# Optimization experiments

Hardware: AMD Instinct MI355X
Metric: run time of the kernel (lower is better)

Reference implementation:

```python
import jax, jax.numpy as jnp
import numpy as np

N = 50000        # nodes
E = 800000       # edges (before self loops)
G = 512          # graphs
H = 2            # heads
FIN = 128        # in_features
CH = 64          # hidden per head
COUT = 32        # out_features
NEG_SLOPE = 0.2  # PyG GATConv default
BN_EPS = 1e-5


def _gat(x, src, dst, W, a_src, a_dst, b, concat, n):
    # x: [n, F], W: [F, H*C], a_src/a_dst: [H, C]
    h = (x @ W).reshape(n, a_src.shape[0], a_src.shape[1])        # [n, H, C]
    e = jax.nn.leaky_relu((h * a_src).sum(-1)[src]
                          + (h * a_dst).sum(-1)[dst], NEG_SLOPE)  # [Etot, H]
    # per-destination segment softmax (self loops guarantee nonempty segments)
    m = jax.ops.segment_max(e, dst, num_segments=n)
    ex = jnp.exp(e - m[dst])
    s = jax.ops.segment_sum(ex, dst, num_segments=n)
    alpha = ex / (s[dst] + 1e-16)                                 # [Etot, H]
    out = jax.ops.segment_sum(h[src] * alpha[:, :, None], dst, num_segments=n)
    out = out.reshape(n, -1) if concat else out.mean(axis=1)
    return out + b


def _bn(x, gamma, beta, mean, var):
    # BatchNorm1d in eval mode (running statistics)
    return (x - mean) * jax.lax.rsqrt(var + BN_EPS) * gamma + beta


def setup_inputs() -> dict:
    key = jax.random.key(0)
    ks = jax.random.split(key, 12)
    x = jax.random.normal(ks[0], (N, FIN), dtype=jnp.float32)
    edge_index = jax.random.randint(ks[1], (2, E), 0, N, dtype=jnp.int32)
    batch = jnp.sort(jax.random.randint(ks[2], (N,), 0, G, dtype=jnp.int32))
    inp = {"x": x, "edge_index": edge_index, "batch": batch}
    # layer 1: GATConv(FIN -> CH, heads=H, concat=True)
    inp["W1"] = jax.random.normal(ks[3], (FIN, H * CH), dtype=jnp.float32) * 0.1
    inp["as1"] = jax.random.normal(ks[4], (H, CH), dtype=jnp.float32) * 0.1
    inp["ad1"] = jax.random.normal(ks[5], (H, CH), dtype=jnp.float32) * 0.1
    inp["b1"] = jnp.zeros((H * CH,), dtype=jnp.float32)
    inp["bn1_gamma"] = jnp.ones((H * CH,), dtype=jnp.float32)
    inp["bn1_beta"] = jnp.zeros((H * CH,), dtype=jnp.float32)
    inp["bn1_mean"] = jax.random.normal(ks[6], (H * CH,), dtype=jnp.float32) * 0.05
    inp["bn1_var"] = jnp.ones((H * CH,), dtype=jnp.float32)
    # layer 2: GATConv(H*CH -> COUT, heads=H, concat=False)
    inp["W2"] = jax.random.normal(ks[7], (H * CH, H * COUT), dtype=jnp.float32) * 0.1
    inp["as2"] = jax.random.normal(ks[8], (H, COUT), dtype=jnp.float32) * 0.1
    inp["ad2"] = jax.random.normal(ks[9], (H, COUT), dtype=jnp.float32) * 0.1
    inp["b2"] = jnp.zeros((COUT,), dtype=jnp.float32)
    inp["bn2_gamma"] = jnp.ones((COUT,), dtype=jnp.float32)
    inp["bn2_beta"] = jnp.zeros((COUT,), dtype=jnp.float32)
    inp["bn2_mean"] = jax.random.normal(ks[10], (COUT,), dtype=jnp.float32) * 0.05
    inp["bn2_var"] = jnp.ones((COUT,), dtype=jnp.float32)
    return inp


def reference(x, edge_index, batch,
              W1, as1, ad1, b1, bn1_gamma, bn1_beta, bn1_mean, bn1_var,
              W2, as2, ad2, b2, bn2_gamma, bn2_beta, bn2_mean, bn2_var):
    n = x.shape[0]
    sl = jnp.arange(n, dtype=edge_index.dtype)
    src = jnp.concatenate([edge_index[0], sl])  # PyG add_self_loops=True
    dst = jnp.concatenate([edge_index[1], sl])
    h = _gat(x, src, dst, W1, as1, ad1, b1, True, n)
    h = jax.nn.relu(_bn(h, bn1_gamma, bn1_beta, bn1_mean, bn1_var))
    h = _gat(h, src, dst, W2, as2, ad2, b2, False, n)
    h = _bn(h, bn2_gamma, bn2_beta, bn2_mean, bn2_var)
    # global mean pool over graphs
    sums = jax.ops.segment_sum(h, batch, num_segments=G)
    cnts = jax.ops.segment_sum(jnp.ones((n,), h.dtype), batch, num_segments=G)
    pooled = sums / jnp.maximum(cnts, 1.0)[:, None]
    return jax.nn.log_softmax(pooled, axis=1)
```

## Files before the change

### kernel.cpp

```cpp
#include <hip/hip_runtime.h>
#include <hip/hip_bf16.h>

#define NEG_SLOPE 0.2f
#define BN_EPS 1e-5f
#define BSHIFT 7
#define P_PART 256
#define MAXB 512

typedef unsigned int uint32;
typedef unsigned short ushort16;
typedef __attribute__((ext_vector_type(8))) short bf16x8;
typedef __attribute__((ext_vector_type(4))) float f32x4;

__device__ __forceinline__ ushort16 f2bf(float f) {
    uint32 u = __float_as_uint(f);
    u = (u + 0x7fff + ((u >> 16) & 1)) >> 16;
    return (ushort16)u;
}
__device__ __forceinline__ float bfu_lo(uint32 u) { return __uint_as_float(u << 16); }
__device__ __forceinline__ float bfu_hi(uint32 u) { return __uint_as_float(u & 0xffff0000u); }

__device__ __forceinline__ void scan_bbase(const int* __restrict__ rowtot, int nbuck,
                                           int Etot, int* sb ) {
    const int t = threadIdx.x;
    int v0 = (t < nbuck) ? rowtot[t] : 0;
    int v1 = (256 + t < nbuck) ? rowtot[256 + t] : 0;
    sb[t] = v0;
    sb[256 + t] = v1;
    __syncthreads();
    for (int off = 1; off < 512; off <<= 1) {
        int a0 = (t >= off) ? sb[t - off] : 0;
        int a1 = (256 + t >= off) ? sb[256 + t - off] : 0;
        __syncthreads();
        sb[t] += a0;
        sb[256 + t] += a1;
        __syncthreads();
    }
    int i0 = sb[t], i1 = sb[256 + t];
    __syncthreads();
    sb[t] = i0 - v0;
    sb[256 + t] = i1 - v1;
    if (t == 0) sb[MAXB] = Etot;
    __syncthreads();
}

template <int OC, int C>
__device__ __forceinline__ void pack_col(int col, int k, const float* __restrict__ W,
                                         const float* __restrict__ a_s,
                                         const float* __restrict__ a_d,
                                         ushort16* __restrict__ wt) {
    float v = 0.f;
    if (col < OC) {
        v = W[k * OC + col];
    } else if (col < OC + 2) {
        int hh = col - OC;
        float s = 0.f;
        for (int c = 0; c < C; ++c) s += W[k * OC + hh * C + c] * a_s[hh * C + c];
        v = s;
    } else if (col < OC + 4) {
        int hh = col - OC - 2;
        float s = 0.f;
        for (int c = 0; c < C; ++c) s += W[k * OC + hh * C + c] * a_d[hh * C + c];
        v = s;
    }
    wt[(size_t)col * 128 + k] = f2bf(v);
}

template <int OC, int NT, bool AF32>
__device__ __forceinline__ void gemm_body(int gb, const void* __restrict__ xin,
                                          const ushort16* __restrict__ wt,
                                          ushort16* __restrict__ h, float4* __restrict__ att,
                                          float2* __restrict__ asc, int N) {
    const int wave = threadIdx.x >> 6, lane = threadIdx.x & 63;
    const int tile = gb * 4 + wave;
    if (tile * 16 >= N) return;
    const int m = lane & 15, quad = lane >> 4;
    const int node = tile * 16 + m;

    bf16x8 a[4];
    if (AF32) {
        const float* xr = (const float*)xin + (size_t)node * 128 + quad * 8;
#pragma unroll
        for (int c = 0; c < 4; ++c) {
            float4 u = *(const float4*)(xr + c * 32);
            float4 v = *(const float4*)(xr + c * 32 + 4);
            bf16x8 t;
            t[0] = (short)f2bf(u.x); t[1] = (short)f2bf(u.y);
            t[2] = (short)f2bf(u.z); t[3] = (short)f2bf(u.w);
            t[4] = (short)f2bf(v.x); t[5] = (short)f2bf(v.y);
            t[6] = (short)f2bf(v.z); t[7] = (short)f2bf(v.w);
            a[c] = t;
        }
    } else {
        const ushort16* xr = (const ushort16*)xin + (size_t)node * 128 + quad * 8;
#pragma unroll
        for (int c = 0; c < 4; ++c) a[c] = *(const bf16x8*)(xr + c * 32);
    }

    for (int t = 0; t < NT; ++t) {
        const ushort16* wr = wt + ((size_t)(t * 16 + m)) * 128 + quad * 8;
        bf16x8 b[4];
#pragma unroll
        for (int c = 0; c < 4; ++c) b[c] = *(const bf16x8*)(wr + c * 32);
        f32x4 acc = {0.f, 0.f, 0.f, 0.f};
#pragma unroll
        for (int c = 0; c < 4; ++c)
            acc = __builtin_amdgcn_mfma_f32_16x16x32_bf16(a[c], b[c], acc, 0, 0, 0);
        if (t * 16 < OC) {
#pragma unroll
            for (int r = 0; r < 4; ++r) {
                int nrow = tile * 16 + quad * 4 + r;
                h[(size_t)nrow * OC + t * 16 + m] = f2bf(acc[r]);
            }
        } else if (m < 4) {
#pragma unroll
            for (int r = 0; r < 4; ++r) {
                int nrow = tile * 16 + quad * 4 + r;
                ((float*)(att + nrow))[m] = acc[r];
                if (m < 2) ((float*)(asc + nrow))[m] = acc[r];
            }
        }
    }
}

__global__ __launch_bounds__(256) void fused_prep(
    const int* __restrict__ ei, int E, int Etot, int nbuck, int chunk, int* __restrict__ hist,
    const float* __restrict__ W1, const float* __restrict__ as1, const float* __restrict__ ad1,
    ushort16* __restrict__ wt1,
    const float* __restrict__ W2, const float* __restrict__ as2, const float* __restrict__ ad2,
    ushort16* __restrict__ wt2,
    const int* __restrict__ batch, int N, int G, int* __restrict__ gstart) {
    const int bid = blockIdx.x;
    if (bid < P_PART) {
        __shared__ int lh[MAXB];
        const int p = bid;
        for (int i = threadIdx.x; i < nbuck; i += 256) lh[i] = 0;
        __syncthreads();
        const int beg = p * chunk;
        const int end = min(beg + chunk, Etot);
        for (int i = beg + threadIdx.x; i < end; i += 256) {
            int d = (i < E) ? ei[E + i] : i - E;
            atomicAdd(&lh[d >> BSHIFT], 1);
        }
        __syncthreads();
        for (int i = threadIdx.x; i < nbuck; i += 256) hist[(size_t)i * P_PART + p] = lh[i];
        return;
    }
    int rb = bid - P_PART;
    if (rb < 72) {
        pack_col<128, 64>(rb * 2 + (threadIdx.x >> 7), threadIdx.x & 127, W1, as1, ad1, wt1);
        return;
    }
    rb -= 72;
    if (rb < 40) {
        pack_col<64, 32>(rb * 2 + (threadIdx.x >> 7), threadIdx.x & 127, W2, as2, ad2, wt2);
        return;
    }
    rb -= 40;
    {
        int g = rb * 256 + (int)threadIdx.x;
        if (g > G) return;
        if (g == G) { gstart[G] = N; return; }
        int lo = 0, hi = N;
        while (lo < hi) { int mid = (lo + hi) >> 1; if (batch[mid] < g) lo = mid + 1; else hi = mid; }
        gstart[g] = lo;
    }
}

__global__ __launch_bounds__(P_PART) void row_scan(int* __restrict__ hist,
                                                   int* __restrict__ rowtot) {
    const int b = blockIdx.x;
    __shared__ int s[P_PART];
    const int t = threadIdx.x;
    int v = hist[(size_t)b * P_PART + t];
    s[t] = v;
    __syncthreads();
    for (int off = 1; off < P_PART; off <<= 1) {
        int u = (t >= off) ? s[t - off] : 0;
        __syncthreads();
        s[t] += u;
        __syncthreads();
    }
    hist[(size_t)b * P_PART + t] = s[t] - v;
    if (t == P_PART - 1) rowtot[b] = s[t];
}

__global__ __launch_bounds__(256) void fused_scatter_gemm1(
    const int* __restrict__ ei, int E, int Etot, int nbuck, int chunk,
    const int* __restrict__ hist, const int* __restrict__ rowtot, uint32* __restrict__ ebuf,
    const void* __restrict__ x, const ushort16* __restrict__ wt1,
    ushort16* __restrict__ h1, float4* __restrict__ att1, float2* __restrict__ asc1, int N) {
    const int bid = blockIdx.x;
    if (bid < P_PART) {
        __shared__ int sb[MAXB + 1];
        __shared__ int cur[MAXB];
        scan_bbase(rowtot, nbuck, Etot, sb);
        const int p = bid;
        for (int i = threadIdx.x; i < nbuck; i += 256)
            cur[i] = sb[i] + hist[(size_t)i * P_PART + p];
        __syncthreads();
        const int beg = p * chunk;
        const int end = min(beg + chunk, Etot);
        for (int i = beg + threadIdx.x; i < end; i += 256) {
            int s_, d_;
            if (i < E) { s_ = ei[i]; d_ = ei[E + i]; }
            else       { s_ = d_ = i - E; }
            int pos = atomicAdd(&cur[d_ >> BSHIFT], 1);
            ebuf[pos] = ((uint32)(d_ & ((1 << BSHIFT) - 1)) << 25) | (uint32)s_;
        }
    } else {
        gemm_body<128, 9, true>(bid - P_PART, x, wt1, h1, att1, asc1, N);
    }
}

__global__ __launch_bounds__(256) void bucket_place(
    const int* __restrict__ rowtot, int nbuck, int Etot, const uint32* __restrict__ ebuf,
    int N, int* __restrict__ base, int* __restrict__ csr_src) {
    const int bk = blockIdx.x;
    __shared__ int sb[MAXB + 1];
    __shared__ int ldeg[1 << BSHIFT];
    __shared__ int sscan[1 << BSHIFT];
    __shared__ int lcur[1 << BSHIFT];
    scan_bbase(rowtot, nbuck, Etot, sb);
    const int t = threadIdx.x;
    if (t < (1 << BSHIFT)) { ldeg[t] = 0; lcur[t] = 0; }
    __syncthreads();
    const int beg = sb[bk], end = sb[bk + 1];
    for (int i = beg + t; i < end; i += 256) atomicAdd(&ldeg[ebuf[i] >> 25], 1);
    __syncthreads();
    if (t < 128) sscan[t] = ldeg[t];
    __syncthreads();
    for (int off = 1; off < 128; off <<= 1) {
        int v = 0;
        if (t < 128 && t >= off) v = sscan[t - off];
        __syncthreads();
        if (t < 128) sscan[t] += v;
        __syncthreads();
    }
    if (t < 128) {
        int node = (bk << BSHIFT) + t;
        if (node < N) base[node] = beg + sscan[t] - ldeg[t];
    }
    __syncthreads();
    for (int i = beg + t; i < end; i += 256) {
        uint32 pk = ebuf[i];
        int dl = (int)(pk >> 25);
        int s_ = (int)(pk & 0x1FFFFFFu);
        int pos = beg + (sscan[dl] - ldeg[dl]) + atomicAdd(&lcur[dl], 1);
        csr_src[pos] = s_;
    }
}

__global__ __launch_bounds__(256) void gemm2_kernel(
    const void* __restrict__ xin, const ushort16* __restrict__ wt,
    ushort16* __restrict__ h, float4* __restrict__ att, float2* __restrict__ asc, int N) {
    gemm_body<64, 5, false>(blockIdx.x, xin, wt, h, att, asc, N);
}

__global__ __launch_bounds__(256) void gat_gather1(
    const int* __restrict__ base, const int* __restrict__ csr_src, int Etot, int N,
    const ushort16* __restrict__ h, const float4* __restrict__ att,
    const float2* __restrict__ asc,
    const float* __restrict__ b, const float* __restrict__ g, const float* __restrict__ be,
    const float* __restrict__ mu, const float* __restrict__ var,
    ushort16* __restrict__ outb) {
    const int node = __builtin_amdgcn_readfirstlane(blockIdx.x * 4 + (threadIdx.x >> 6));
    if (node >= N) return;
    const int t = threadIdx.x & 63;
    const int sub = t >> 4;
    const int q = t & 15;
    const int hh = q >> 3;
    const int beg = base[node];
    const int end = (node + 1 < N) ? base[node + 1] : Etot;
    const int deg = end - beg;
    const float4 adn = att[node];

    float a0 = 0.f, a1 = 0.f, a2 = 0.f, a3 = 0.f;
    float a4 = 0.f, a5 = 0.f, a6 = 0.f, a7 = 0.f;
    float ssum0 = 0.f, ssum1 = 0.f;

    for (int c0e = 0; c0e < deg; c0e += 64) {
        const int rel = c0e + t;
        const bool ok = rel < deg;
        const int sidxme = csr_src[beg + (ok ? rel : 0)];
        const float2 av = asc[sidxme];
        float e0 = av.x + adn.z, e1 = av.y + adn.w;
        e0 = e0 > 0.f ? e0 : NEG_SLOPE * e0;
        e1 = e1 > 0.f ? e1 : NEG_SLOPE * e1;
        const float x0 = ok ? __expf(e0) : 0.f;
        const float x1 = ok ? __expf(e1) : 0.f;
        float r0 = x0, r1 = x1;
#pragma unroll
        for (int off = 1; off < 64; off <<= 1) {
            r0 += __shfl_xor(r0, off, 64);
            r1 += __shfl_xor(r1, off, 64);
        }
        ssum0 += r0;
        ssum1 += r1;
        const int degc = min(deg - c0e, 64);
        const int kkmax = (degc + 3) >> 2;
        for (int kk = 0; kk < kkmax; kk += 4) {
            int sidx[4];
            float exv[4];
            uint4 hv[4];
#pragma unroll
            for (int j = 0; j < 4; ++j) {
                const int s = 4 * (kk + j) + sub;
                const bool v = s < degc;
                sidx[j] = __shfl(sidxme, s, 64);
                float f0 = __shfl(x0, s, 64);
                float f1 = __shfl(x1, s, 64);
                exv[j] = v ? (hh ? f1 : f0) : 0.f;
                hv[j] = v ? *(const uint4*)(h + (size_t)sidx[j] * 128 + 8 * q)
                          : make_uint4(0u, 0u, 0u, 0u);
            }
#pragma unroll
            for (int j = 0; j < 4; ++j) {
                const float ex = exv[j];
                a0 += ex * bfu_lo(hv[j].x);
                a1 += ex * bfu_hi(hv[j].x);
                a2 += ex * bfu_lo(hv[j].y);
                a3 += ex * bfu_hi(hv[j].y);
                a4 += ex * bfu_lo(hv[j].z);
                a5 += ex * bfu_hi(hv[j].z);
                a6 += ex * bfu_lo(hv[j].w);
                a7 += ex * bfu_hi(hv[j].w);
            }
        }
    }
#pragma unroll
    for (int off = 16; off <= 32; off <<= 1) {
        a0 += __shfl_xor(a0, off, 64);
        a1 += __shfl_xor(a1, off, 64);
        a2 += __shfl_xor(a2, off, 64);
        a3 += __shfl_xor(a3, off, 64);
        a4 += __shfl_xor(a4, off, 64);
        a5 += __shfl_xor(a5, off, 64);
        a6 += __shfl_xor(a6, off, 64);
        a7 += __shfl_xor(a7, off, 64);
    }
    if (t < 16) {
        const float inv = 1.f / ((hh ? ssum1 : ssum0) + 1e-16f);
        const int c0 = 8 * q;
        float va[8] = {a0, a1, a2, a3, a4, a5, a6, a7};
        uint32 pk[4];
#pragma unroll
        for (int i = 0; i < 8; i += 2) {
            float v0 = va[i] * inv + b[c0 + i];
            float v1 = va[i + 1] * inv + b[c0 + i + 1];
            v0 = fmaxf((v0 - mu[c0 + i]) * rsqrtf(var[c0 + i] + BN_EPS) * g[c0 + i] + be[c0 + i], 0.f);
            v1 = fmaxf((v1 - mu[c0 + i + 1]) * rsqrtf(var[c0 + i + 1] + BN_EPS) * g[c0 + i + 1] + be[c0 + i + 1], 0.f);
            pk[i >> 1] = (uint32)f2bf(v0) | ((uint32)f2bf(v1) << 16);
        }
        uint4 r = make_uint4(pk[0], pk[1], pk[2], pk[3]);
        *(uint4*)(outb + (size_t)node * 128 + c0) = r;
    }
}

__global__ __launch_bounds__(256) void gat_gather2(
    const int* __restrict__ base, const int* __restrict__ csr_src, int Etot, int N,
    const ushort16* __restrict__ h2, const float4* __restrict__ att,
    const float2* __restrict__ asc,
    const float* __restrict__ b2, const float* __restrict__ g, const float* __restrict__ be,
    const float* __restrict__ mu, const float* __restrict__ var,
    float* __restrict__ node_out) {
    const int node = __builtin_amdgcn_readfirstlane(blockIdx.x * 4 + (threadIdx.x >> 6));
    if (node >= N) return;
    const int t = threadIdx.x & 63;
    const int sub = t >> 4;
    const int q = t & 15;
    const int hh = q >> 3;
    const int beg = base[node];
    const int end = (node + 1 < N) ? base[node + 1] : Etot;
    const int deg = end - beg;
    const float4 adn = att[node];

    float a0 = 0.f, a1 = 0.f, a2 = 0.f, a3 = 0.f;
    float ssum0 = 0.f, ssum1 = 0.f;

    for (int c0e = 0; c0e < deg; c0e += 64) {
        const int rel = c0e + t;
        const bool ok = rel < deg;
        const int sidxme = csr_src[beg + (ok ? rel : 0)];
        const float2 av = asc[sidxme];
        float e0 = av.x + adn.z, e1 = av.y + adn.w;
        e0 = e0 > 0.f ? e0 : NEG_SLOPE * e0;
        e1 = e1 > 0.f ? e1 : NEG_SLOPE * e1;
        const float x0 = ok ? __expf(e0) : 0.f;
        const float x1 = ok ? __expf(e1) : 0.f;
        float r0 = x0, r1 = x1;
#pragma unroll
        for (int off = 1; off < 64; off <<= 1) {
            r0 += __shfl_xor(r0, off, 64);
            r1 += __shfl_xor(r1, off, 64);
        }
        ssum0 += r0;
        ssum1 += r1;
        const int degc = min(deg - c0e, 64);
        const int kkmax = (degc + 3) >> 2;
        for (int kk = 0; kk < kkmax; kk += 4) {
            int sidx[4];
            float exv[4];
            uint2 hv[4];
#pragma unroll
            for (int j = 0; j < 4; ++j) {
                const int s = 4 * (kk + j) + sub;
                const bool v = s < degc;
                sidx[j] = __shfl(sidxme, s, 64);
                float f0 = __shfl(x0, s, 64);
                float f1 = __shfl(x1, s, 64);
                exv[j] = v ? (hh ? f1 : f0) : 0.f;
                hv[j] = v ? *(const uint2*)(h2 + (size_t)sidx[j] * 64 + 4 * q)
                          : make_uint2(0u, 0u);
            }
#pragma unroll
            for (int j = 0; j < 4; ++j) {
                const float ex = exv[j];
                a0 += ex * bfu_lo(hv[j].x);
                a1 += ex * bfu_hi(hv[j].x);
                a2 += ex * bfu_lo(hv[j].y);
                a3 += ex * bfu_hi(hv[j].y);
            }
        }
    }
#pragma unroll
    for (int off = 16; off <= 32; off <<= 1) {
        a0 += __shfl_xor(a0, off, 64);
        a1 += __shfl_xor(a1, off, 64);
        a2 += __shfl_xor(a2, off, 64);
        a3 += __shfl_xor(a3, off, 64);
    }
    const float inv = 1.f / ((hh ? ssum1 : ssum0) + 1e-16f);
    float v0 = a0 * inv, v1 = a1 * inv, v2 = a2 * inv, v3 = a3 * inv;
    const int src = (t & 15) + 8;
    float p0 = __shfl(v0, src, 64);
    float p1 = __shfl(v1, src, 64);
    float p2 = __shfl(v2, src, 64);
    float p3 = __shfl(v3, src, 64);
    if (t < 8) {
        const int c0 = 4 * t;
        float m0 = 0.5f * (v0 + p0) + b2[c0];
        float m1 = 0.5f * (v1 + p1) + b2[c0 + 1];
        float m2 = 0.5f * (v2 + p2) + b2[c0 + 2];
        float m3 = 0.5f * (v3 + p3) + b2[c0 + 3];
        m0 = (m0 - mu[c0]) * rsqrtf(var[c0] + BN_EPS) * g[c0] + be[c0];
        m1 = (m1 - mu[c0 + 1]) * rsqrtf(var[c0 + 1] + BN_EPS) * g[c0 + 1] + be[c0 + 1];
        m2 = (m2 - mu[c0 + 2]) * rsqrtf(var[c0 + 2] + BN_EPS) * g[c0 + 2] + be[c0 + 2];
        m3 = (m3 - mu[c0 + 3]) * rsqrtf(var[c0 + 3] + BN_EPS) * g[c0 + 3] + be[c0 + 3];
        *(float4*)(node_out + (size_t)node * 32 + c0) = make_float4(m0, m1, m2, m3);
    }
}

__global__ __launch_bounds__(256) void pool_logsoftmax(
    const float* __restrict__ node_out, const int* __restrict__ gstart,
    float* __restrict__ out) {
    const int gidx = blockIdx.x;
    const int tid = threadIdx.x;
    const int c = tid & 31, r = tid >> 5;
    const int n0 = gstart[gidx], n1 = gstart[gidx + 1];
    float s = 0.f;
    for (int n = n0 + r; n < n1; n += 8) s += node_out[(size_t)n * 32 + c];
    __shared__ float red[8][32];
    red[r][c] = s;
    __syncthreads();
    if (r == 0) {
        float tot = red[0][c];
#pragma unroll
        for (int k = 1; k < 8; ++k) tot += red[k][c];
        float v = tot / fmaxf((float)(n1 - n0), 1.f);
        float m = v;
#pragma unroll
        for (int off = 16; off >= 1; off >>= 1) m = fmaxf(m, __shfl_xor(m, off, 64));
        float ex = __expf(v - m);
        float ssum = ex;
#pragma unroll
        for (int off = 16; off >= 1; off >>= 1) ssum += __shfl_xor(ssum, off, 64);
        out[gidx * 32 + c] = v - m - logf(ssum);
    }
}

extern "C" void kernel_launch(void* const* d_in, const int* in_sizes, int n_in,
                              void* d_out, int out_size, void* d_ws, size_t ws_size,
                              hipStream_t stream) {
    const float* x   = (const float*)d_in[0];
    const int* ei    = (const int*)d_in[1];
    const int* batch = (const int*)d_in[2];
    const float* W1  = (const float*)d_in[3];
    const float* as1 = (const float*)d_in[4];
    const float* ad1 = (const float*)d_in[5];
    const float* b1  = (const float*)d_in[6];
    const float* g1  = (const float*)d_in[7];
    const float* be1 = (const float*)d_in[8];
    const float* mu1 = (const float*)d_in[9];
    const float* vr1 = (const float*)d_in[10];
    const float* W2  = (const float*)d_in[11];
    const float* as2 = (const float*)d_in[12];
    const float* ad2 = (const float*)d_in[13];
    const float* b2  = (const float*)d_in[14];
    const float* g2  = (const float*)d_in[15];
    const float* be2 = (const float*)d_in[16];
    const float* mu2 = (const float*)d_in[17];
    const float* vr2 = (const float*)d_in[18];
    float* out = (float*)d_out;

    const int N = in_sizes[0] / 128;
    const int E = in_sizes[1] / 2;
    const int Etot = E + N;
    const int G = out_size / 32;
    const int nbuck = (N + (1 << BSHIFT) - 1) >> BSHIFT;
    const int chunk = (Etot + P_PART - 1) / P_PART;
    const int M = nbuck * P_PART;
    const int ntile = (N + 15) / 16;
    const int gemm_grid = (ntile + 3) / 4;
    const int gbb = (G + 1 + 255) / 256;

    float* p = (float*)d_ws;
    size_t o = 0;
    auto al = [&]() { o = (o + 3) & ~(size_t)3; };
    ushort16* h1b   = (ushort16*)(p + o); o += (size_t)N * 64;  al();
    ushort16* agg1b = (ushort16*)(p + o); o += (size_t)N * 64;  al();
    ushort16* h2b   = (ushort16*)(p + o); o += (size_t)N * 32;  al();
    float4* att1 = (float4*)(p + o); o += (size_t)N * 4;  al();
    float4* att2 = (float4*)(p + o); o += (size_t)N * 4;  al();
    float2* asc1 = (float2*)(p + o); o += (size_t)N * 2;  al();
    float2* asc2 = (float2*)(p + o); o += (size_t)N * 2;  al();
    float* nodeo = p + o; o += (size_t)N * 32; al();
    ushort16* wt1 = (ushort16*)(p + o); o += (size_t)144 * 64; al();
    ushort16* wt2 = (ushort16*)(p + o); o += (size_t)80 * 64;  al();
    int* csr_src = (int*)(p + o); o += (size_t)Etot; al();
    uint32* ebuf = (uint32*)(p + o); o += (size_t)Etot; al();
    int* base    = (int*)(p + o); o += (size_t)N;    al();
    int* hist    = (int*)(p + o); o += (size_t)M;    al();
    int* rowtot  = (int*)(p + o); o += (size_t)nbuck + 4; al();
    int* gstart  = (int*)(p + o); o += (size_t)G + 4; al();

    fused_prep<<<P_PART + 72 + 40 + gbb, 256, 0, stream>>>(
        ei, E, Etot, nbuck, chunk, hist, W1, as1, ad1, wt1, W2, as2, ad2, wt2,
        batch, N, G, gstart);
    row_scan<<<nbuck, P_PART, 0, stream>>>(hist, rowtot);
    fused_scatter_gemm1<<<P_PART + gemm_grid, 256, 0, stream>>>(
        ei, E, Etot, nbuck, chunk, hist, rowtot, ebuf, x, wt1, h1b, att1, asc1, N);
    bucket_place<<<nbuck, 256, 0, stream>>>(rowtot, nbuck, Etot, ebuf, N, base, csr_src);
    gat_gather1<<<(N + 3) / 4, 256, 0, stream>>>(base, csr_src, Etot, N, h1b, att1, asc1,
                                                 b1, g1, be1, mu1, vr1, agg1b);
    gemm2_kernel<<<gemm_grid, 256, 0, stream>>>(agg1b, wt2, h2b, att2, asc2, N);
    gat_gather2<<<(N + 3) / 4, 256, 0, stream>>>(base, csr_src, Etot, N, h2b, att2, asc2,
                                                 b2, g2, be2, mu2, vr2, nodeo);
    pool_logsoftmax<<<G, 256, 0, stream>>>(nodeo, gstart, out);
}
```

Before: 234.0 us.

## Assign one node per 16-lane group in GAT gathers and precompute BN affine

Both gather kernels now give each destination node a 16-lane group instead of a full 64-lane wavefront, so a block handles 16 nodes rather than 4. The softmax reductions run over 16-lane chunks, and the cross-subgroup accumulator reduction is gone. The aim is to stop idling lanes on low-degree nodes, since the average degree is about 17. Bias plus batch-norm is folded into a per-channel scale and shift computed once in the prep kernel, which removes repeated rsqrt and parameter loads per node. The trade-off is more divergence between lanes in a wavefront when node degrees differ, and less memory-level parallelism per node.

```diff
diff --git a/kernel.cpp b/kernel.cpp
--- a/kernel.cpp
+++ b/kernel.cpp
@@ -129,6 +129,11 @@
     ushort16* __restrict__ wt1,
     const float* __restrict__ W2, const float* __restrict__ as2, const float* __restrict__ ad2,
     ushort16* __restrict__ wt2,
+    const float* __restrict__ b1, const float* __restrict__ g1, const float* __restrict__ be1,
+    const float* __restrict__ mu1, const float* __restrict__ vr1,
+    const float* __restrict__ b2, const float* __restrict__ g2, const float* __restrict__ be2,
+    const float* __restrict__ mu2, const float* __restrict__ vr2,
+    float2* __restrict__ bn1, float2* __restrict__ bn2,
     const int* __restrict__ batch, int N, int G, int* __restrict__ gstart) {
     const int bid = blockIdx.x;
     if (bid < P_PART) {
@@ -157,6 +162,19 @@
         return;
     }
     rb -= 40;
+    if (rb == 0) {
+        const int c = threadIdx.x;
+        if (c < 128) {
+            float A = g1[c] * rsqrtf(vr1[c] + BN_EPS);
+            bn1[c] = make_float2(A, A * (b1[c] - mu1[c]) + be1[c]);
+        } else if (c < 160) {
+            const int c2 = c - 128;
+            float A = g2[c2] * rsqrtf(vr2[c2] + BN_EPS);
+            bn2[c2] = make_float2(A, A * (b2[c2] - mu2[c2]) + be2[c2]);
+        }
+        return;
+    }
+    rb -= 1;
     {
         int g = rb * 256 + (int)threadIdx.x;
         if (g > G) return;
@@ -260,15 +278,14 @@
 __global__ __launch_bounds__(256) void gat_gather1(
     const int* __restrict__ base, const int* __restrict__ csr_src, int Etot, int N,
     const ushort16* __restrict__ h, const float4* __restrict__ att,
-    const float2* __restrict__ asc,
-    const float* __restrict__ b, const float* __restrict__ g, const float* __restrict__ be,
-    const float* __restrict__ mu, const float* __restrict__ var,
+    const float2* __restrict__ asc, const float2* __restrict__ bn1,
     ushort16* __restrict__ outb) {
-    const int node = __builtin_amdgcn_readfirstlane(blockIdx.x * 4 + (threadIdx.x >> 6));
+    const int tid = threadIdx.x;
+    const int node = blockIdx.x * 16 + (tid >> 4);
     if (node >= N) return;
-    const int t = threadIdx.x & 63;
-    const int sub = t >> 4;
-    const int q = t & 15;
+    const int t = tid & 63;
+    const int q = tid & 15;
+    const int gbase = t & 48;
     const int hh = q >> 3;
     const int beg = base[node];
     const int end = (node + 1 < N) ? base[node + 1] : Etot;
@@ -279,10 +296,10 @@
     float a4 = 0.f, a5 = 0.f, a6 = 0.f, a7 = 0.f;
     float ssum0 = 0.f, ssum1 = 0.f;
 
-    for (int c0e = 0; c0e < deg; c0e += 64) {
-        const int rel = c0e + t;
-        const bool ok = rel < deg;
-        const int sidxme = csr_src[beg + (ok ? rel : 0)];
+    for (int c0e = 0; c0e < deg; c0e += 16) {
+        const int degc = min(deg - c0e, 16);
+        const bool ok = q < degc;
+        const int sidxme = csr_src[beg + c0e + (ok ? q : 0)];
         const float2 av = asc[sidxme];
         float e0 = av.x + adn.z, e1 = av.y + adn.w;
         e0 = e0 > 0.f ? e0 : NEG_SLOPE * e0;
@@ -291,25 +308,24 @@
         const float x1 = ok ? __expf(e1) : 0.f;
         float r0 = x0, r1 = x1;
 #pragma unroll
-        for (int off = 1; off < 64; off <<= 1) {
-            r0 += __shfl_xor(r0, off, 64);
-            r1 += __shfl_xor(r1, off, 64);
+        for (int off = 1; off < 16; off <<= 1) {
+            r0 += __shfl_xor(r0, off, 16);
+            r1 += __shfl_xor(r1, off, 16);
         }
         ssum0 += r0;
         ssum1 += r1;
-        const int degc = min(deg - c0e, 64);
-        const int kkmax = (degc + 3) >> 2;
-        for (int kk = 0; kk < kkmax; kk += 4) {
+        for (int e = 0; e < degc; e += 4) {
             int sidx[4];
             float exv[4];
             uint4 hv[4];
 #pragma unroll
             for (int j = 0; j < 4; ++j) {
-                const int s = 4 * (kk + j) + sub;
+                const int s = e + j;
                 const bool v = s < degc;
-                sidx[j] = __shfl(sidxme, s, 64);
-                float f0 = __shfl(x0, s, 64);
-                float f1 = __shfl(x1, s, 64);
+                const int sl = gbase + s;
+                sidx[j] = __shfl(sidxme, sl, 64);
+                float f0 = __shfl(x0, sl, 64);
+                float f1 = __shfl(x1, sl, 64);
                 exv[j] = v ? (hh ? f1 : f0) : 0.f;
                 hv[j] = v ? *(const uint4*)(h + (size_t)sidx[j] * 128 + 8 * q)
                           : make_uint4(0u, 0u, 0u, 0u);
@@ -328,47 +344,34 @@
             }
         }
     }
-#pragma unroll
-    for (int off = 16; off <= 32; off <<= 1) {
-        a0 += __shfl_xor(a0, off, 64);
-        a1 += __shfl_xor(a1, off, 64);
-        a2 += __shfl_xor(a2, off, 64);
-        a3 += __shfl_xor(a3, off, 64);
-        a4 += __shfl_xor(a4, off, 64);
-        a5 += __shfl_xor(a5, off, 64);
-        a6 += __shfl_xor(a6, off, 64);
-        a7 += __shfl_xor(a7, off, 64);
-    }
-    if (t < 16) {
-        const float inv = 1.f / ((hh ? ssum1 : ssum0) + 1e-16f);
-        const int c0 = 8 * q;
-        float va[8] = {a0, a1, a2, a3, a4, a5, a6, a7};
-        uint32 pk[4];
-#pragma unroll
-        for (int i = 0; i < 8; i += 2) {
-            float v0 = va[i] * inv + b[c0 + i];
-            float v1 = va[i + 1] * inv + b[c0 + i + 1];
-            v0 = fmaxf((v0 - mu[c0 + i]) * rsqrtf(var[c0 + i] + BN_EPS) * g[c0 + i] + be[c0 + i], 0.f);
-            v1 = fmaxf((v1 - mu[c0 + i + 1]) * rsqrtf(var[c0 + i + 1] + BN_EPS) * g[c0 + i + 1] + be[c0 + i + 1], 0.f);
-            pk[i >> 1] = (uint32)f2bf(v0) | ((uint32)f2bf(v1) << 16);
-        }
-        uint4 r = make_uint4(pk[0], pk[1], pk[2], pk[3]);
-        *(uint4*)(outb + (size_t)node * 128 + c0) = r;
-    }
+    const float inv = 1.f / ((hh ? ssum1 : ssum0) + 1e-16f);
+    const int c0 = 8 * q;
+    const float4* bp = (const float4*)(bn1 + c0);
+    const float4 w0 = bp[0], w1 = bp[1], w2 = bp[2], w3 = bp[3];
+    float va[8] = {a0, a1, a2, a3, a4, a5, a6, a7};
+    float Ac[8] = {w0.x, w0.z, w1.x, w1.z, w2.x, w2.z, w3.x, w3.z};
+    float Cc[8] = {w0.y, w0.w, w1.y, w1.w, w2.y, w2.w, w3.y, w3.w};
+    uint32 pk[4];
+#pragma unroll
+    for (int i = 0; i < 8; i += 2) {
+        float v0 = fmaxf(fmaf(Ac[i], va[i] * inv, Cc[i]), 0.f);
+        float v1 = fmaxf(fmaf(Ac[i + 1], va[i + 1] * inv, Cc[i + 1]), 0.f);
+        pk[i >> 1] = (uint32)f2bf(v0) | ((uint32)f2bf(v1) << 16);
+    }
+    *(uint4*)(outb + (size_t)node * 128 + c0) = make_uint4(pk[0], pk[1], pk[2], pk[3]);
 }
 
 __global__ __launch_bounds__(256) void gat_gather2(
     const int* __restrict__ base, const int* __restrict__ csr_src, int Etot, int N,
     const ushort16* __restrict__ h2, const float4* __restrict__ att,
-    const float2* __restrict__ asc,
-    const float* __restrict__ b2, const float* __restrict__ g, const float* __restrict__ be,
-    const float* __restrict__ mu, const float* __restrict__ var,
+    const float2* __restrict__ asc, const float2* __restrict__ bn2,
     float* __restrict__ node_out) {
-    const int node = __builtin_amdgcn_readfirstlane(blockIdx.x * 4 + (threadIdx.x >> 6));
+    const int tid = threadIdx.x;
+    const int node = blockIdx.x * 16 + (tid >> 4);
     if (node >= N) return;
-    const int t = threadIdx.x & 63;
-    const int sub = t >> 4;
-    const int q = t & 15;
+    const int t = tid & 63;
+    const int q = tid & 15;
+    const int gbase = t & 48;
     const int hh = q >> 3;
     const int beg = base[node];
     const int end = (node + 1 < N) ? base[node + 1] : Etot;
@@ -378,10 +381,10 @@
     float a0 = 0.f, a1 = 0.f, a2 = 0.f, a3 = 0.f;
     float ssum0 = 0.f, ssum1 = 0.f;
 
-    for (int c0e = 0; c0e < deg; c0e += 64) {
-        const int rel = c0e + t;
-        const bool ok = rel < deg;
-        const int sidxme = csr_src[beg + (ok ? rel : 0)];
+    for (int c0e = 0; c0e < deg; c0e += 16) {
+        const int degc = min(deg - c0e, 16);
+        const bool ok = q < degc;
+        const int sidxme = csr_src[beg + c0e + (ok ? q : 0)];
         const float2 av = asc[sidxme];
         float e0 = av.x + adn.z, e1 = av.y + adn.w;
         e0 = e0 > 0.f ? e0 : NEG_SLOPE * e0;
@@ -390,25 +393,24 @@
         const float x1 = ok ? __expf(e1) : 0.f;
         float r0 = x0, r1 = x1;
 #pragma unroll
-        for (int off = 1; off < 64; off <<= 1) {
-            r0 += __shfl_xor(r0, off, 64);
-            r1 += __shfl_xor(r1, off, 64);
+        for (int off = 1; off < 16; off <<= 1) {
+            r0 += __shfl_xor(r0, off, 16);
+            r1 += __shfl_xor(r1, off, 16);
         }
         ssum0 += r0;
         ssum1 += r1;
-        const int degc = min(deg - c0e, 64);
-        const int kkmax = (degc + 3) >> 2;
-        for (int kk = 0; kk < kkmax; kk += 4) {
+        for (int e = 0; e < degc; e += 4) {
             int sidx[4];
             float exv[4];
             uint2 hv[4];
 #pragma unroll
             for (int j = 0; j < 4; ++j) {
-                const int s = 4 * (kk + j) + sub;
+                const int s = e + j;
                 const bool v = s < degc;
-                sidx[j] = __shfl(sidxme, s, 64);
-                float f0 = __shfl(x0, s, 64);
-                float f1 = __shfl(x1, s, 64);
+                const int sl = gbase + s;
+                sidx[j] = __shfl(sidxme, sl, 64);
+                float f0 = __shfl(x0, sl, 64);
+                float f1 = __shfl(x1, sl, 64);
                 exv[j] = v ? (hh ? f1 : f0) : 0.f;
                 hv[j] = v ? *(const uint2*)(h2 + (size_t)sidx[j] * 64 + 4 * q)
                           : make_uint2(0u, 0u);
@@ -423,30 +425,21 @@
             }
         }
     }
-#pragma unroll
-    for (int off = 16; off <= 32; off <<= 1) {
-        a0 += __shfl_xor(a0, off, 64);
-        a1 += __shfl_xor(a1, off, 64);
-        a2 += __shfl_xor(a2, off, 64);
-        a3 += __shfl_xor(a3, off, 64);
-    }
     const float inv = 1.f / ((hh ? ssum1 : ssum0) + 1e-16f);
     float v0 = a0 * inv, v1 = a1 * inv, v2 = a2 * inv, v3 = a3 * inv;
-    const int src = (t & 15) + 8;
-    float p0 = __shfl(v0, src, 64);
-    float p1 = __shfl(v1, src, 64);
-    float p2 = __shfl(v2, src, 64);
-    float p3 = __shfl(v3, src, 64);
-    if (t < 8) {
-        const int c0 = 4 * t;
-        float m0 = 0.5f * (v0 + p0) + b2[c0];
-        float m1 = 0.5f * (v1 + p1) + b2[c0 + 1];
-        float m2 = 0.5f * (v2 + p2) + b2[c0 + 2];
-        float m3 = 0.5f * (v3 + p3) + b2[c0 + 3];
-        m0 = (m0 - mu[c0]) * rsqrtf(var[c0] + BN_EPS) * g[c0] + be[c0];
-        m1 = (m1 - mu[c0 + 1]) * rsqrtf(var[c0 + 1] + BN_EPS) * g[c0 + 1] + be[c0 + 1];
-        m2 = (m2 - mu[c0 + 2]) * rsqrtf(var[c0 + 2] + BN_EPS) * g[c0 + 2] + be[c0 + 2];
-        m3 = (m3 - mu[c0 + 3]) * rsqrtf(var[c0 + 3] + BN_EPS) * g[c0 + 3] + be[c0 + 3];
+    const int psrc = gbase | ((q + 8) & 15);
+    float p0 = __shfl(v0, psrc, 64);
+    float p1 = __shfl(v1, psrc, 64);
+    float p2 = __shfl(v2, psrc, 64);
+    float p3 = __shfl(v3, psrc, 64);
+    if (q < 8) {
+        const int c0 = 4 * q;
+        const float4* bp = (const float4*)(bn2 + c0);
+        const float4 w0 = bp[0], w1 = bp[1];
+        float m0 = fmaf(w0.x, 0.5f * (v0 + p0), w0.y);
+        float m1 = fmaf(w0.z, 0.5f * (v1 + p1), w0.w);
+        float m2 = fmaf(w1.x, 0.5f * (v2 + p2), w1.y);
+        float m3 = fmaf(w1.z, 0.5f * (v3 + p3), w1.w);
         *(float4*)(node_out + (size_t)node * 32 + c0) = make_float4(m0, m1, m2, m3);
     }
 }
@@ -527,6 +520,8 @@
     float* nodeo = p + o; o += (size_t)N * 32; al();
     ushort16* wt1 = (ushort16*)(p + o); o += (size_t)144 * 64; al();
     ushort16* wt2 = (ushort16*)(p + o); o += (size_t)80 * 64;  al();
+    float2* bn1  = (float2*)(p + o); o += (size_t)128 * 2; al();
+    float2* bn2  = (float2*)(p + o); o += (size_t)32 * 2;  al();
     int* csr_src = (int*)(p + o); o += (size_t)Etot; al();
     uint32* ebuf = (uint32*)(p + o); o += (size_t)Etot; al();
     int* base    = (int*)(p + o); o += (size_t)N;    al();
@@ -534,17 +529,18 @@
     int* rowtot  = (int*)(p + o); o += (size_t)nbuck + 4; al();
     int* gstart  = (int*)(p + o); o += (size_t)G + 4; al();
 
-    fused_prep<<<P_PART + 72 + 40 + gbb, 256, 0, stream>>>(
+    fused_prep<<<P_PART + 72 + 40 + 1 + gbb, 256, 0, stream>>>(
         ei, E, Etot, nbuck, chunk, hist, W1, as1, ad1, wt1, W2, as2, ad2, wt2,
+        b1, g1, be1, mu1, vr1, b2, g2, be2, mu2, vr2, bn1, bn2,
         batch, N, G, gstart);
     row_scan<<<nbuck, P_PART, 0, stream>>>(hist, rowtot);
     fused_scatter_gemm1<<<P_PART + gemm_grid, 256, 0, stream>>>(
         ei, E, Etot, nbuck, chunk, hist, rowtot, ebuf, x, wt1, h1b, att1, asc1, N);
     bucket_place<<<nbuck, 256, 0, stream>>>(rowtot, nbuck, Etot, ebuf, N, base, csr_src);
-    gat_gather1<<<(N + 3) / 4, 256, 0, stream>>>(base, csr_src, Etot, N, h1b, att1, asc1,
-                                                 b1, g1, be1, mu1, vr1, agg1b);
+    gat_gather1<<<(N + 15) / 16, 256, 0, stream>>>(base, csr_src, Etot, N, h1b, att1, asc1,
+                                                   bn1, agg1b);
     gemm2_kernel<<<gemm_grid, 256, 0, stream>>>(agg1b, wt2, h2b, att2, asc2, N);
-    gat_gather2<<<(N + 3) / 4, 256, 0, stream>>>(base, csr_src, Etot, N, h2b, att2, asc2,
-                                                 b2, g2, be2, mu2, vr2, nodeo);
+    gat_gather2<<<(N + 15) / 16, 256, 0, stream>>>(base, csr_src, Etot, N, h2b, att2, asc2,
+                                                   bn2, nodeo);
     pool_logsoftmax<<<G, 256, 0, stream>>>(nodeo, gstart, out);
 }
```

Result: faster. 222.1 us (-5.1%).
